# Optimization experiments

Hardware: AMD Instinct MI355X
Metric: run time of the kernel (lower is better)

Reference implementation:

```python
import jax, jax.numpy as jnp
import numpy as np

B, S, H = 2, 4096, 256
NH, NKV = 8, 4
HD = H // NH          # 32
GROUPS = NH // NKV    # 2
ROPE_BASE = 10000.0


def _rope_cos_sin(seq_len, dim, dtype):
    inv_freq = 1.0 / (ROPE_BASE ** (jnp.arange(0, dim, 2, dtype=jnp.float32) / dim))
    t = jnp.arange(seq_len, dtype=jnp.float32)
    freqs = jnp.outer(t, inv_freq)            # [S, dim/2]
    emb = jnp.concatenate([freqs, freqs], -1)  # [S, dim]
    return jnp.cos(emb).astype(dtype), jnp.sin(emb).astype(dtype)


def _rotate_half(x):
    x1, x2 = jnp.split(x, 2, axis=-1)
    return jnp.concatenate([-x2, x1], axis=-1)


def setup_inputs() -> dict:
    key = jax.random.key(0)
    k0, k1, k2, k3, k4 = jax.random.split(key, 5)
    return {
        "hidden_states": jax.random.normal(k0, (B, S, H), jnp.float32),
        "Wq": jax.random.normal(k1, (H, H), jnp.float32) * 0.02,
        "Wk": jax.random.normal(k2, (NKV * HD, H), jnp.float32) * 0.02,
        "Wv": jax.random.normal(k3, (NKV * HD, H), jnp.float32) * 0.02,
        "Wo": jax.random.normal(k4, (H, H), jnp.float32) * 0.02,
    }


def reference(hidden_states, Wq, Wk, Wv, Wo):
    b, s, _ = hidden_states.shape
    # projections (nn.Linear: x @ W.T)
    q = (hidden_states @ Wq.T).reshape(b, s, NH, HD).transpose(0, 2, 1, 3)   # [b,nh,s,hd]
    k = (hidden_states @ Wk.T).reshape(b, s, NKV, HD).transpose(0, 2, 1, 3)  # [b,nkv,s,hd]
    v = (hidden_states @ Wv.T).reshape(b, s, NKV, HD).transpose(0, 2, 1, 3)
    # RoPE
    cos, sin = _rope_cos_sin(s, HD, hidden_states.dtype)  # [s,hd]
    q = q * cos + _rotate_half(q) * sin
    k = k * cos + _rotate_half(k) * sin
    # GQA: repeat kv heads (repeat_interleave over head dim)
    k = jnp.repeat(k, GROUPS, axis=1)  # [b,nh,s,hd]
    v = jnp.repeat(v, GROUPS, axis=1)
    # scores + causal mask
    scores = jnp.einsum('bhqd,bhkd->bhqk', q, k) / jnp.sqrt(jnp.float32(HD)).astype(q.dtype)
    causal = jnp.triu(jnp.full((s, s), -jnp.inf, dtype=scores.dtype), k=1)
    scores = scores + causal
    attn = jax.nn.softmax(scores.astype(jnp.float32), axis=-1).astype(q.dtype)
    out = jnp.einsum('bhqk,bhkd->bhqd', attn, v)          # [b,nh,s,hd]
    out = out.transpose(0, 2, 1, 3).reshape(b, s, NH * HD)
    return out @ Wo.T
```

## Files before the change

kernel.cpp:

```cpp
#include <hip/hip_runtime.h>
#include <hip/hip_bf16.h>
#include <stdint.h>

#define NB 2
#define SEQ 4096
#define HID 256
#define NHEAD 8
#define NKVH 4
#define HDIM 32

typedef __bf16 bf16;
typedef __bf16 bf16x8 __attribute__((ext_vector_type(8)));
typedef float f32x4 __attribute__((ext_vector_type(4)));

static __device__ __forceinline__ uint16_t bfbits(float f) {
    bf16 h = (bf16)f;
    return __builtin_bit_cast(uint16_t, h);
}
static __device__ __forceinline__ uint32_t pack_bf16(float lo, float hi) {
    return (uint32_t)bfbits(lo) | ((uint32_t)bfbits(hi) << 16);
}
static __device__ __forceinline__ float fexp2(float x) {
#if __has_builtin(__builtin_amdgcn_exp2f)
    return __builtin_amdgcn_exp2f(x);
#else
    float r; asm("v_exp_f32 %0, %1" : "=v"(r) : "v"(x)); return r;
#endif
}
static __device__ __forceinline__ void gld_lds16(const void* g, void* l) {
    __builtin_amdgcn_global_load_lds(
        (const __attribute__((address_space(1))) void*)g,
        (__attribute__((address_space(3))) void*)l, 16, 0, 0);
}

__global__ __launch_bounds__(256) void to_bf16(
    const float* __restrict__ hs, const float* __restrict__ Wq,
    const float* __restrict__ Wk, const float* __restrict__ Wv,
    const float* __restrict__ Wo,
    bf16* __restrict__ hsb, bf16* __restrict__ Wb, bf16* __restrict__ Wob)
{
    size_t idx = ((size_t)blockIdx.x * 256 + threadIdx.x) * 8;
    const float* src; bf16* dst; size_t off;
    if (idx < 2097152)      { src = hs; dst = hsb;        off = idx; }
    else if (idx < 2162688) { src = Wq; dst = Wb;         off = idx - 2097152; }
    else if (idx < 2195456) { src = Wk; dst = Wb + 65536; off = idx - 2162688; }
    else if (idx < 2228224) { src = Wv; dst = Wb + 98304; off = idx - 2195456; }
    else                    { src = Wo; dst = Wob;        off = idx - 2228224; }
    float4 a = *(const float4*)&src[off];
    float4 b = *(const float4*)&src[off + 4];
    uint32_t u0 = pack_bf16(a.x, a.y);
    uint32_t u1 = pack_bf16(a.z, a.w);
    uint32_t u2 = pack_bf16(b.x, b.y);
    uint32_t u3 = pack_bf16(b.z, b.w);
    *(uint4*)&dst[off] = make_uint4(u0, u1, u2, u3);
}

__global__ __launch_bounds__(256, 2) void qkv2(
    const bf16* __restrict__ hsb, const bf16* __restrict__ Wb,
    bf16* __restrict__ qws, bf16* __restrict__ kws, bf16* __restrict__ vtws)
{
    __shared__ bf16 As[64 * 256];
    __shared__ bf16 Bs[64 * 256];
    const int t = threadIdx.x;
    const int wid = t >> 6, lane = t & 63;
    const int g = lane >> 4, c = lane & 15;
    const int n0 = blockIdx.x * 64;
    const int m0 = blockIdx.y * 64;

    {
        const int half = lane >> 5;
        const int seg = lane & 31;
        #pragma unroll
        for (int i = 0; i < 8; ++i) {
            const int row = (i * 4 + wid) * 2 + half;
            const int sseg = seg ^ (row & 7);
            gld_lds16(hsb + (size_t)(m0 + row) * 256 + sseg * 8,
                      (char*)As + wid * 1024 + i * 4096);
            gld_lds16(Wb + (size_t)(n0 + row) * 256 + sseg * 8,
                      (char*)Bs + wid * 1024 + i * 4096);
        }
    }
    __syncthreads();

    const f32x4 zf = {0.f, 0.f, 0.f, 0.f};
    f32x4 acc[4] = {zf, zf, zf, zf};
    const int r = wid * 16 + c;
    const int aBase = r * 512;
    const int s7 = c & 7;
    #pragma unroll
    for (int j = 0; j < 8; ++j) {
        const int so = ((4 * j + g) ^ s7) << 4;
        bf16x8 af = *(const bf16x8*)((const char*)As + aBase + so);
        #pragma unroll
        for (int nt = 0; nt < 4; ++nt) {
            bf16x8 bfr = *(const bf16x8*)((const char*)Bs + (nt * 16 + c) * 512 + so);
            acc[nt] = __builtin_amdgcn_mfma_f32_16x16x32_bf16(af, bfr, acc[nt], 0, 0, 0);
        }
    }

    const float qscale = 1.4426950408889634f * 0.17677669529663687f;
    const float invf = exp2f(-0.83048202372184f * (float)c);
    #pragma unroll
    for (int rr = 0; rr < 4; ++rr) {
        int m = m0 + wid * 16 + g * 4 + rr;
        int b = m >> 12, s = m & (SEQ - 1);
        float sn, cs;
        sincosf((float)s * invf, &sn, &cs);
        if (n0 < 256) {
            #pragma unroll
            for (int np = 0; np < 4; np += 2) {
                int h = (n0 + np * 16) >> 5;
                float x1 = acc[np][rr], x2 = acc[np + 1][rr];
                float y1 = (x1 * cs - x2 * sn) * qscale;
                float y2 = (x2 * cs + x1 * sn) * qscale;
                size_t base = ((size_t)(b * NHEAD + h) * SEQ + s) * HDIM;
                qws[base + c] = (bf16)y1;
                qws[base + 16 + c] = (bf16)y2;
            }
        } else if (n0 < 384) {
            #pragma unroll
            for (int np = 0; np < 4; np += 2) {
                int kh = (n0 - 256 + np * 16) >> 5;
                float x1 = acc[np][rr], x2 = acc[np + 1][rr];
                float y1 = x1 * cs - x2 * sn;
                float y2 = x2 * cs + x1 * sn;
                size_t base = ((size_t)(b * NKVH + kh) * SEQ + s) * HDIM;
                kws[base + c] = (bf16)y1;
                kws[base + 16 + c] = (bf16)y2;
            }
        } else {
            #pragma unroll
            for (int nt = 0; nt < 4; ++nt) {
                int ng = n0 + nt * 16 + c - 384;
                int vh = ng >> 5, d = ng & 31;
                vtws[((size_t)(b * NKVH + vh) * HDIM + d) * SEQ + s] = (bf16)acc[nt][rr];
            }
        }
    }
}

__global__ __launch_bounds__(256, 2) void attn_fwd(
    const bf16* __restrict__ qws, const bf16* __restrict__ kws,
    const bf16* __restrict__ vtws,
    float* __restrict__ Oa, float* __restrict__ Ob,
    float* __restrict__ la, float* __restrict__ lb)
{
    __shared__ bf16 Kb[2][64 * 32];
    __shared__ bf16 Vb[2][32 * 64];
    __shared__ float tr[4][16 * 33];
    const int t = threadIdx.x;
    const int w = t >> 6, lane = t & 63;
    const int g = lane >> 4, c = lane & 15;
    const int wg = blockIdx.x;
    const int h = wg & 7;
    const int rest = wg >> 3;
    const int half = rest & 1;
    const int r2 = rest >> 1;
    const int b = r2 & 1;
    const int T = 31 - (r2 >> 1);
    const int kvh = h >> 1;
    const bf16* Kg = kws + (size_t)(b * NKVH + kvh) * SEQ * HDIM;
    const bf16* Vg = vtws + (size_t)(b * NKVH + kvh) * HDIM * SEQ;
    const int cbase = half * (T + 1);
    const int nloc = T + 1;
    const int q0 = T * 128 + w * 32;
    const int d_w = 2 * T + (w >> 1);

    const bf16* Qb = qws + (size_t)(b * NHEAD + h) * SEQ * HDIM;
    bf16x8 qf0 = *(const bf16x8*)&Qb[(size_t)(q0 + c) * HDIM + g * 8];
    bf16x8 qf1 = *(const bf16x8*)&Qb[(size_t)(q0 + 16 + c) * HDIM + g * 8];

    const int sd = t >> 3, sseg = t & 7;
    const bf16* kg_t = Kg + t * 8;
    const bf16* vg_t = Vg + (size_t)sd * SEQ + (sseg ^ (sd & 7)) * 8;
    char* kl[2] = { (char*)&Kb[0][0] + w * 1024, (char*)&Kb[1][0] + w * 1024 };
    char* vl[2] = { (char*)&Vb[0][0] + w * 1024, (char*)&Vb[1][0] + w * 1024 };

    const int kperm = 8 * (c >> 2) + (c & 3);
    const int kro = kperm * 64 + g * 16;
    const int cx = c & 7;
    const int vro0 = c * 128, vro1 = (16 + c) * 128;

    const f32x4 zf = {0.f, 0.f, 0.f, 0.f};
    union { uint32_t u[4]; bf16x8 v; } onesf;
    onesf.u[0] = onesf.u[1] = onesf.u[2] = onesf.u[3] = 0x3F803F80u;

    f32x4 o00 = zf, o01 = zf, ol0 = zf;
    f32x4 o10 = zf, o11 = zf, ol1 = zf;

    gld_lds16(kg_t + (size_t)cbase * 2048, kl[0]);
    gld_lds16(vg_t + (size_t)cbase * 64, vl[0]);
    __syncthreads();

    #pragma unroll 1
    for (int s = 0; s < nloc; ++s) {
        const int ci = cbase + s;
        const int sn = s + 1;
        if (sn < nloc) {
            gld_lds16(kg_t + (size_t)(cbase + sn) * 2048, kl[sn & 1]);
            gld_lds16(vg_t + (size_t)(cbase + sn) * 64, vl[sn & 1]);
        }
        if (ci <= d_w) {
            const char* kbuf = (const char*)&Kb[s & 1][0];
            const char* vbuf = (const char*)&Vb[s & 1][0];

            bf16x8 kf0 = *(const bf16x8*)(kbuf + kro);
            bf16x8 kf1 = *(const bf16x8*)(kbuf + kro + 256);
            bf16x8 kf2 = *(const bf16x8*)(kbuf + kro + 2048);
            bf16x8 kf3 = *(const bf16x8*)(kbuf + kro + 2304);
            bf16x8 vf00 = *(const bf16x8*)(vbuf + vro0 + ((g ^ cx) << 4));
            bf16x8 vf01 = *(const bf16x8*)(vbuf + vro1 + ((g ^ cx) << 4));
            bf16x8 vf10 = *(const bf16x8*)(vbuf + vro0 + (((4 + g) ^ cx) << 4));
            bf16x8 vf11 = *(const bf16x8*)(vbuf + vro1 + (((4 + g) ^ cx) << 4));

            const bool diag = (ci == d_w);
            const int qbase = (w & 1) * 32 + c;

            {
                f32x4 st0 = __builtin_amdgcn_mfma_f32_16x16x32_bf16(kf0, qf0, zf, 0, 0, 0);
                f32x4 st1 = __builtin_amdgcn_mfma_f32_16x16x32_bf16(kf1, qf0, zf, 0, 0, 0);
                f32x4 st2 = __builtin_amdgcn_mfma_f32_16x16x32_bf16(kf2, qf0, zf, 0, 0, 0);
                f32x4 st3 = __builtin_amdgcn_mfma_f32_16x16x32_bf16(kf3, qf0, zf, 0, 0, 0);
                if (diag) {
                    const int qoff = qbase;
                    #pragma unroll
                    for (int rr = 0; rr < 4; ++rr) {
                        if (8 * g + rr > qoff)          st0[rr] = -1e30f;
                        if (8 * g + 4 + rr > qoff)      st1[rr] = -1e30f;
                        if (32 + 8 * g + rr > qoff)     st2[rr] = -1e30f;
                        if (32 + 8 * g + 4 + rr > qoff) st3[rr] = -1e30f;
                    }
                }
                float p00 = fexp2(st0[0]), p01 = fexp2(st0[1]), p02 = fexp2(st0[2]), p03 = fexp2(st0[3]);
                float p10 = fexp2(st1[0]), p11 = fexp2(st1[1]), p12 = fexp2(st1[2]), p13 = fexp2(st1[3]);
                float p20 = fexp2(st2[0]), p21 = fexp2(st2[1]), p22 = fexp2(st2[2]), p23 = fexp2(st2[3]);
                float p30 = fexp2(st3[0]), p31 = fexp2(st3[1]), p32 = fexp2(st3[2]), p33 = fexp2(st3[3]);
                union { uint32_t u[4]; bf16x8 v; } pb0, pb1;
                asm("v_cvt_pk_bf16_f32 %0, %1, %2" : "=v"(pb0.u[0]) : "v"(p00), "v"(p01));
                asm("v_cvt_pk_bf16_f32 %0, %1, %2" : "=v"(pb0.u[1]) : "v"(p02), "v"(p03));
                asm("v_cvt_pk_bf16_f32 %0, %1, %2" : "=v"(pb0.u[2]) : "v"(p10), "v"(p11));
                asm("v_cvt_pk_bf16_f32 %0, %1, %2" : "=v"(pb0.u[3]) : "v"(p12), "v"(p13));
                asm("v_cvt_pk_bf16_f32 %0, %1, %2" : "=v"(pb1.u[0]) : "v"(p20), "v"(p21));
                asm("v_cvt_pk_bf16_f32 %0, %1, %2" : "=v"(pb1.u[1]) : "v"(p22), "v"(p23));
                asm("v_cvt_pk_bf16_f32 %0, %1, %2" : "=v"(pb1.u[2]) : "v"(p30), "v"(p31));
                asm("v_cvt_pk_bf16_f32 %0, %1, %2" : "=v"(pb1.u[3]) : "v"(p32), "v"(p33));
                o00 = __builtin_amdgcn_mfma_f32_16x16x32_bf16(vf00, pb0.v, o00, 0, 0, 0);
                o01 = __builtin_amdgcn_mfma_f32_16x16x32_bf16(vf01, pb0.v, o01, 0, 0, 0);
                ol0 = __builtin_amdgcn_mfma_f32_16x16x32_bf16(onesf.v, pb0.v, ol0, 0, 0, 0);
                o00 = __builtin_amdgcn_mfma_f32_16x16x32_bf16(vf10, pb1.v, o00, 0, 0, 0);
                o01 = __builtin_amdgcn_mfma_f32_16x16x32_bf16(vf11, pb1.v, o01, 0, 0, 0);
                ol0 = __builtin_amdgcn_mfma_f32_16x16x32_bf16(onesf.v, pb1.v, ol0, 0, 0, 0);
            }
            {
                f32x4 st0 = __builtin_amdgcn_mfma_f32_16x16x32_bf16(kf0, qf1, zf, 0, 0, 0);
                f32x4 st1 = __builtin_amdgcn_mfma_f32_16x16x32_bf16(kf1, qf1, zf, 0, 0, 0);
                f32x4 st2 = __builtin_amdgcn_mfma_f32_16x16x32_bf16(kf2, qf1, zf, 0, 0, 0);
                f32x4 st3 = __builtin_amdgcn_mfma_f32_16x16x32_bf16(kf3, qf1, zf, 0, 0, 0);
                if (diag) {
                    const int qoff = qbase + 16;
                    #pragma unroll
                    for (int rr = 0; rr < 4; ++rr) {
                        if (8 * g + rr > qoff)          st0[rr] = -1e30f;
                        if (8 * g + 4 + rr > qoff)      st1[rr] = -1e30f;
                        if (32 + 8 * g + rr > qoff)     st2[rr] = -1e30f;
                        if (32 + 8 * g + 4 + rr > qoff) st3[rr] = -1e30f;
                    }
                }
                float p00 = fexp2(st0[0]), p01 = fexp2(st0[1]), p02 = fexp2(st0[2]), p03 = fexp2(st0[3]);
                float p10 = fexp2(st1[0]), p11 = fexp2(st1[1]), p12 = fexp2(st1[2]), p13 = fexp2(st1[3]);
                float p20 = fexp2(st2[0]), p21 = fexp2(st2[1]), p22 = fexp2(st2[2]), p23 = fexp2(st2[3]);
                float p30 = fexp2(st3[0]), p31 = fexp2(st3[1]), p32 = fexp2(st3[2]), p33 = fexp2(st3[3]);
                union { uint32_t u[4]; bf16x8 v; } pb0, pb1;
                asm("v_cvt_pk_bf16_f32 %0, %1, %2" : "=v"(pb0.u[0]) : "v"(p00), "v"(p01));
                asm("v_cvt_pk_bf16_f32 %0, %1, %2" : "=v"(pb0.u[1]) : "v"(p02), "v"(p03));
                asm("v_cvt_pk_bf16_f32 %0, %1, %2" : "=v"(pb0.u[2]) : "v"(p10), "v"(p11));
                asm("v_cvt_pk_bf16_f32 %0, %1, %2" : "=v"(pb0.u[3]) : "v"(p12), "v"(p13));
                asm("v_cvt_pk_bf16_f32 %0, %1, %2" : "=v"(pb1.u[0]) : "v"(p20), "v"(p21));
                asm("v_cvt_pk_bf16_f32 %0, %1, %2" : "=v"(pb1.u[1]) : "v"(p22), "v"(p23));
                asm("v_cvt_pk_bf16_f32 %0, %1, %2" : "=v"(pb1.u[2]) : "v"(p30), "v"(p31));
                asm("v_cvt_pk_bf16_f32 %0, %1, %2" : "=v"(pb1.u[3]) : "v"(p32), "v"(p33));
                o10 = __builtin_amdgcn_mfma_f32_16x16x32_bf16(vf00, pb0.v, o10, 0, 0, 0);
                o11 = __builtin_amdgcn_mfma_f32_16x16x32_bf16(vf01, pb0.v, o11, 0, 0, 0);
                ol1 = __builtin_amdgcn_mfma_f32_16x16x32_bf16(onesf.v, pb0.v, ol1, 0, 0, 0);
                o10 = __builtin_amdgcn_mfma_f32_16x16x32_bf16(vf10, pb1.v, o10, 0, 0, 0);
                o11 = __builtin_amdgcn_mfma_f32_16x16x32_bf16(vf11, pb1.v, o11, 0, 0, 0);
                ol1 = __builtin_amdgcn_mfma_f32_16x16x32_bf16(onesf.v, pb1.v, ol1, 0, 0, 0);
            }
        }
        __syncthreads();
    }

    #pragma unroll 1
    for (int j = 0; j < 2; ++j) {
        f32x4 a0 = j ? o10 : o00;
        f32x4 a1 = j ? o11 : o01;
        f32x4 al = j ? ol1 : ol0;
        #pragma unroll
        for (int rr = 0; rr < 4; ++rr) {
            tr[w][c * 33 + 4 * g + rr]      = a0[rr];
            tr[w][c * 33 + 16 + 4 * g + rr] = a1[rr];
        }
        float* Op = half ? Ob : Oa;
        float* lp = half ? lb : la;
        if (g == 0) lp[((size_t)b * SEQ + q0 + j * 16 + c) * 8 + h] = al[0];
        int q = lane >> 2, dp = (lane & 3) * 8;
        size_t m = (size_t)b * SEQ + q0 + j * 16 + q;
        float4 f0 = make_float4(tr[w][q * 33 + dp + 0], tr[w][q * 33 + dp + 1],
                                tr[w][q * 33 + dp + 2], tr[w][q * 33 + dp + 3]);
        float4 f1 = make_float4(tr[w][q * 33 + dp + 4], tr[w][q * 33 + dp + 5],
                                tr[w][q * 33 + dp + 6], tr[w][q * 33 + dp + 7]);
        *(float4*)&Op[m * HID + h * HDIM + dp]     = f0;
        *(float4*)&Op[m * HID + h * HDIM + dp + 4] = f1;
    }
}

__global__ __launch_bounds__(256) void combine(
    const float* __restrict__ Oa, const float* __restrict__ Ob,
    const float* __restrict__ la, const float* __restrict__ lb,
    bf16* __restrict__ att)
{
    const size_t e = ((size_t)blockIdx.x * 256 + threadIdx.x) * 8;
    const size_t m = e >> 8;
    const int hh = (int)(e & 255) >> 5;
    const float inv = 1.0f / (la[m * 8 + hh] + lb[m * 8 + hh]);
    float4 a0 = *(const float4*)&Oa[e];
    float4 a1 = *(const float4*)&Oa[e + 4];
    float4 b0 = *(const float4*)&Ob[e];
    float4 b1 = *(const float4*)&Ob[e + 4];
    uint32_t u0 = pack_bf16((a0.x + b0.x) * inv, (a0.y + b0.y) * inv);
    uint32_t u1 = pack_bf16((a0.z + b0.z) * inv, (a0.w + b0.w) * inv);
    uint32_t u2 = pack_bf16((a1.x + b1.x) * inv, (a1.y + b1.y) * inv);
    uint32_t u3 = pack_bf16((a1.z + b1.z) * inv, (a1.w + b1.w) * inv);
    *(uint4*)&att[e] = make_uint4(u0, u1, u2, u3);
}

__global__ __launch_bounds__(256, 2) void out_proj2(
    const bf16* __restrict__ att, const bf16* __restrict__ Wob,
    float* __restrict__ out)
{
    __shared__ bf16 As[64 * 256];
    __shared__ bf16 Bs[64 * 256];
    const int t = threadIdx.x;
    const int wid = t >> 6, lane = t & 63;
    const int g = lane >> 4, c = lane & 15;
    const int n0 = blockIdx.x * 64;
    const int m0 = blockIdx.y * 64;

    {
        const int half = lane >> 5;
        const int seg = lane & 31;
        #pragma unroll
        for (int i = 0; i < 8; ++i) {
            const int row = (i * 4 + wid) * 2 + half;
            const int sseg = seg ^ (row & 7);
            gld_lds16(att + (size_t)(m0 + row) * 256 + sseg * 8,
                      (char*)As + wid * 1024 + i * 4096);
            gld_lds16(Wob + (size_t)(n0 + row) * 256 + sseg * 8,
                      (char*)Bs + wid * 1024 + i * 4096);
        }
    }
    __syncthreads();

    const f32x4 zf = {0.f, 0.f, 0.f, 0.f};
    f32x4 acc[4] = {zf, zf, zf, zf};
    const int r = wid * 16 + c;
    const int aBase = r * 512;
    const int s7 = c & 7;
    #pragma unroll
    for (int j = 0; j < 8; ++j) {
        const int so = ((4 * j + g) ^ s7) << 4;
        bf16x8 af = *(const bf16x8*)((const char*)As + aBase + so);
        #pragma unroll
        for (int nt = 0; nt < 4; ++nt) {
            bf16x8 bfr = *(const bf16x8*)((const char*)Bs + (nt * 16 + c) * 512 + so);
            acc[nt] = __builtin_amdgcn_mfma_f32_16x16x32_bf16(af, bfr, acc[nt], 0, 0, 0);
        }
    }

    #pragma unroll
    for (int nt = 0; nt < 4; ++nt) {
        #pragma unroll
        for (int rr = 0; rr < 4; ++rr) {
            int m = m0 + wid * 16 + g * 4 + rr;
            out[(size_t)m * HID + n0 + nt * 16 + c] = acc[nt][rr];
        }
    }
}

extern "C" void kernel_launch(void* const* d_in, const int* in_sizes, int n_in,
                              void* d_out, int out_size, void* d_ws, size_t ws_size,
                              hipStream_t stream) {
    const float* hs = (const float*)d_in[0];
    const float* Wq = (const float*)d_in[1];
    const float* Wk = (const float*)d_in[2];
    const float* Wv = (const float*)d_in[3];
    const float* Wo = (const float*)d_in[4];
    char* ws = (char*)d_ws;
    bf16* qws  = (bf16*)(ws);
    bf16* kws  = (bf16*)(ws + 4194304);
    bf16* vtws = (bf16*)(ws + 6291456);
    bf16* att  = (bf16*)(ws + 8388608);
    float* Oa  = (float*)(ws + 12582912);
    float* Ob  = (float*)(ws + 20971520);
    float* la  = (float*)(ws + 29360128);
    float* lb  = (float*)(ws + 29622272);
    bf16* hsb  = (bf16*)(ws + 29884416);
    bf16* Wb   = (bf16*)(ws + 34078720);
    bf16* Wob  = (bf16*)(ws + 34340864);

    to_bf16<<<1120, 256, 0, stream>>>(hs, Wq, Wk, Wv, Wo, hsb, Wb, Wob);
    qkv2<<<dim3(8, 128), 256, 0, stream>>>(hsb, Wb, qws, kws, vtws);
    attn_fwd<<<1024, 256, 0, stream>>>(qws, kws, vtws, Oa, Ob, la, lb);
    combine<<<1024, 256, 0, stream>>>(Oa, Ob, la, lb, att);
    out_proj2<<<dim3(4, 128), 256, 0, stream>>>(att, Wob, (float*)d_out);
}
```

Measured before the change: 62.93 us.

## Use four-stage LDS ring and process two KV chunks per barrier in attention

Replaces the double-buffered K/V staging with a four-slot ring in a single 32KB shared buffer, prefetching two chunks ahead and processing two chunks per loop iteration so only one __syncthreads is paid per pair of chunks. The per-chunk compute is moved into a macro invoked twice per iteration. The epilogue transpose scratch now aliases the K region of the shared buffer. This deepens prefetch and halves barrier count at the cost of doubling LDS from 16KB to 32KB of K/V staging, which may reduce occupancy.

```diff
diff --git a/kernel.cpp b/kernel.cpp
--- a/kernel.cpp
+++ b/kernel.cpp
@@ -139,15 +139,99 @@
     }
 }
 
+#define ATT_CHUNK(CI, KBUF, VBUF)                                              \
+  do {                                                                         \
+    const char* kbuf = (KBUF);                                                 \
+    const char* vbuf = (VBUF);                                                 \
+    bf16x8 kf0 = *(const bf16x8*)(kbuf + kro);                                 \
+    bf16x8 kf1 = *(const bf16x8*)(kbuf + kro + 256);                           \
+    bf16x8 kf2 = *(const bf16x8*)(kbuf + kro + 2048);                          \
+    bf16x8 kf3 = *(const bf16x8*)(kbuf + kro + 2304);                          \
+    bf16x8 vf00 = *(const bf16x8*)(vbuf + vro0 + ((g ^ cx) << 4));             \
+    bf16x8 vf01 = *(const bf16x8*)(vbuf + vro1 + ((g ^ cx) << 4));             \
+    bf16x8 vf10 = *(const bf16x8*)(vbuf + vro0 + (((4 + g) ^ cx) << 4));       \
+    bf16x8 vf11 = *(const bf16x8*)(vbuf + vro1 + (((4 + g) ^ cx) << 4));       \
+    const bool diag = ((CI) == d_w);                                           \
+    const int qbase = (w & 1) * 32 + c;                                        \
+    {                                                                          \
+        f32x4 st0 = __builtin_amdgcn_mfma_f32_16x16x32_bf16(kf0, qf0, zf, 0, 0, 0); \
+        f32x4 st1 = __builtin_amdgcn_mfma_f32_16x16x32_bf16(kf1, qf0, zf, 0, 0, 0); \
+        f32x4 st2 = __builtin_amdgcn_mfma_f32_16x16x32_bf16(kf2, qf0, zf, 0, 0, 0); \
+        f32x4 st3 = __builtin_amdgcn_mfma_f32_16x16x32_bf16(kf3, qf0, zf, 0, 0, 0); \
+        if (diag) {                                                            \
+            const int qoff = qbase;                                            \
+            _Pragma("unroll")                                                  \
+            for (int rr = 0; rr < 4; ++rr) {                                   \
+                if (8 * g + rr > qoff)          st0[rr] = -1e30f;              \
+                if (8 * g + 4 + rr > qoff)      st1[rr] = -1e30f;              \
+                if (32 + 8 * g + rr > qoff)     st2[rr] = -1e30f;              \
+                if (32 + 8 * g + 4 + rr > qoff) st3[rr] = -1e30f;              \
+            }                                                                  \
+        }                                                                      \
+        float p00 = fexp2(st0[0]), p01 = fexp2(st0[1]), p02 = fexp2(st0[2]), p03 = fexp2(st0[3]); \
+        float p10 = fexp2(st1[0]), p11 = fexp2(st1[1]), p12 = fexp2(st1[2]), p13 = fexp2(st1[3]); \
+        float p20 = fexp2(st2[0]), p21 = fexp2(st2[1]), p22 = fexp2(st2[2]), p23 = fexp2(st2[3]); \
+        float p30 = fexp2(st3[0]), p31 = fexp2(st3[1]), p32 = fexp2(st3[2]), p33 = fexp2(st3[3]); \
+        union { uint32_t u[4]; bf16x8 v; } pb0, pb1;                           \
+        asm("v_cvt_pk_bf16_f32 %0, %1, %2" : "=v"(pb0.u[0]) : "v"(p00), "v"(p01)); \
+        asm("v_cvt_pk_bf16_f32 %0, %1, %2" : "=v"(pb0.u[1]) : "v"(p02), "v"(p03)); \
+        asm("v_cvt_pk_bf16_f32 %0, %1, %2" : "=v"(pb0.u[2]) : "v"(p10), "v"(p11)); \
+        asm("v_cvt_pk_bf16_f32 %0, %1, %2" : "=v"(pb0.u[3]) : "v"(p12), "v"(p13)); \
+        asm("v_cvt_pk_bf16_f32 %0, %1, %2" : "=v"(pb1.u[0]) : "v"(p20), "v"(p21)); \
+        asm("v_cvt_pk_bf16_f32 %0, %1, %2" : "=v"(pb1.u[1]) : "v"(p22), "v"(p23)); \
+        asm("v_cvt_pk_bf16_f32 %0, %1, %2" : "=v"(pb1.u[2]) : "v"(p30), "v"(p31)); \
+        asm("v_cvt_pk_bf16_f32 %0, %1, %2" : "=v"(pb1.u[3]) : "v"(p32), "v"(p33)); \
+        o00 = __builtin_amdgcn_mfma_f32_16x16x32_bf16(vf00, pb0.v, o00, 0, 0, 0); \
+        o01 = __builtin_amdgcn_mfma_f32_16x16x32_bf16(vf01, pb0.v, o01, 0, 0, 0); \
+        ol0 = __builtin_amdgcn_mfma_f32_16x16x32_bf16(onesf.v, pb0.v, ol0, 0, 0, 0); \
+        o00 = __builtin_amdgcn_mfma_f32_16x16x32_bf16(vf10, pb1.v, o00, 0, 0, 0); \
+        o01 = __builtin_amdgcn_mfma_f32_16x16x32_bf16(vf11, pb1.v, o01, 0, 0, 0); \
+        ol0 = __builtin_amdgcn_mfma_f32_16x16x32_bf16(onesf.v, pb1.v, ol0, 0, 0, 0); \
+    }                                                                          \
+    {                                                                          \
+        f32x4 st0 = __builtin_amdgcn_mfma_f32_16x16x32_bf16(kf0, qf1, zf, 0, 0, 0); \
+        f32x4 st1 = __builtin_amdgcn_mfma_f32_16x16x32_bf16(kf1, qf1, zf, 0, 0, 0); \
+        f32x4 st2 = __builtin_amdgcn_mfma_f32_16x16x32_bf16(kf2, qf1, zf, 0, 0, 0); \
+        f32x4 st3 = __builtin_amdgcn_mfma_f32_16x16x32_bf16(kf3, qf1, zf, 0, 0, 0); \
+        if (diag) {                                                            \
+            const int qoff = qbase + 16;                                       \
+            _Pragma("unroll")                                                  \
+            for (int rr = 0; rr < 4; ++rr) {                                   \
+                if (8 * g + rr > qoff)          st0[rr] = -1e30f;              \
+                if (8 * g + 4 + rr > qoff)      st1[rr] = -1e30f;              \
+                if (32 + 8 * g + rr > qoff)     st2[rr] = -1e30f;              \
+                if (32 + 8 * g + 4 + rr > qoff) st3[rr] = -1e30f;              \
+            }                                                                  \
+        }                                                                      \
+        float p00 = fexp2(st0[0]), p01 = fexp2(st0[1]), p02 = fexp2(st0[2]), p03 = fexp2(st0[3]); \
+        float p10 = fexp2(st1[0]), p11 = fexp2(st1[1]), p12 = fexp2(st1[2]), p13 = fexp2(st1[3]); \
+        float p20 = fexp2(st2[0]), p21 = fexp2(st2[1]), p22 = fexp2(st2[2]), p23 = fexp2(st2[3]); \
+        float p30 = fexp2(st3[0]), p31 = fexp2(st3[1]), p32 = fexp2(st3[2]), p33 = fexp2(st3[3]); \
+        union { uint32_t u[4]; bf16x8 v; } pb0, pb1;                           \
+        asm("v_cvt_pk_bf16_f32 %0, %1, %2" : "=v"(pb0.u[0]) : "v"(p00), "v"(p01)); \
+        asm("v_cvt_pk_bf16_f32 %0, %1, %2" : "=v"(pb0.u[1]) : "v"(p02), "v"(p03)); \
+        asm("v_cvt_pk_bf16_f32 %0, %1, %2" : "=v"(pb0.u[2]) : "v"(p10), "v"(p11)); \
+        asm("v_cvt_pk_bf16_f32 %0, %1, %2" : "=v"(pb0.u[3]) : "v"(p12), "v"(p13)); \
+        asm("v_cvt_pk_bf16_f32 %0, %1, %2" : "=v"(pb1.u[0]) : "v"(p20), "v"(p21)); \
+        asm("v_cvt_pk_bf16_f32 %0, %1, %2" : "=v"(pb1.u[1]) : "v"(p22), "v"(p23)); \
+        asm("v_cvt_pk_bf16_f32 %0, %1, %2" : "=v"(pb1.u[2]) : "v"(p30), "v"(p31)); \
+        asm("v_cvt_pk_bf16_f32 %0, %1, %2" : "=v"(pb1.u[3]) : "v"(p32), "v"(p33)); \
+        o10 = __builtin_amdgcn_mfma_f32_16x16x32_bf16(vf00, pb0.v, o10, 0, 0, 0); \
+        o11 = __builtin_amdgcn_mfma_f32_16x16x32_bf16(vf01, pb0.v, o11, 0, 0, 0); \
+        ol1 = __builtin_amdgcn_mfma_f32_16x16x32_bf16(onesf.v, pb0.v, ol1, 0, 0, 0); \
+        o10 = __builtin_amdgcn_mfma_f32_16x16x32_bf16(vf10, pb1.v, o10, 0, 0, 0); \
+        o11 = __builtin_amdgcn_mfma_f32_16x16x32_bf16(vf11, pb1.v, o11, 0, 0, 0); \
+        ol1 = __builtin_amdgcn_mfma_f32_16x16x32_bf16(onesf.v, pb1.v, ol1, 0, 0, 0); \
+    }                                                                          \
+  } while (0)
+
 __global__ __launch_bounds__(256, 2) void attn_fwd(
     const bf16* __restrict__ qws, const bf16* __restrict__ kws,
     const bf16* __restrict__ vtws,
     float* __restrict__ Oa, float* __restrict__ Ob,
     float* __restrict__ la, float* __restrict__ lb)
 {
-    __shared__ bf16 Kb[2][64 * 32];
-    __shared__ bf16 Vb[2][32 * 64];
-    __shared__ float tr[4][16 * 33];
+    __shared__ char smem[32768];
     const int t = threadIdx.x;
     const int w = t >> 6, lane = t & 63;
     const int g = lane >> 4, c = lane & 15;
@@ -173,8 +257,8 @@
     const int sd = t >> 3, sseg = t & 7;
     const bf16* kg_t = Kg + t * 8;
     const bf16* vg_t = Vg + (size_t)sd * SEQ + (sseg ^ (sd & 7)) * 8;
-    char* kl[2] = { (char*)&Kb[0][0] + w * 1024, (char*)&Kb[1][0] + w * 1024 };
-    char* vl[2] = { (char*)&Vb[0][0] + w * 1024, (char*)&Vb[1][0] + w * 1024 };
+    char* kl = smem + w * 1024;
+    char* vl = smem + 16384 + w * 1024;
 
     const int kperm = 8 * (c >> 2) + (c & 3);
     const int kro = kperm * 64 + g * 16;
@@ -188,108 +272,42 @@
     f32x4 o00 = zf, o01 = zf, ol0 = zf;
     f32x4 o10 = zf, o11 = zf, ol1 = zf;
 
-    gld_lds16(kg_t + (size_t)cbase * 2048, kl[0]);
-    gld_lds16(vg_t + (size_t)cbase * 64, vl[0]);
+    gld_lds16(kg_t + (size_t)cbase * 2048, kl);
+    gld_lds16(vg_t + (size_t)cbase * 64, vl);
+    if (1 < nloc) {
+        gld_lds16(kg_t + (size_t)(cbase + 1) * 2048, kl + 4096);
+        gld_lds16(vg_t + (size_t)(cbase + 1) * 64, vl + 4096);
+    }
     __syncthreads();
 
+    const int nit = (nloc + 1) >> 1;
     #pragma unroll 1
-    for (int s = 0; s < nloc; ++s) {
-        const int ci = cbase + s;
-        const int sn = s + 1;
-        if (sn < nloc) {
-            gld_lds16(kg_t + (size_t)(cbase + sn) * 2048, kl[sn & 1]);
-            gld_lds16(vg_t + (size_t)(cbase + sn) * 64, vl[sn & 1]);
-        }
-        if (ci <= d_w) {
-            const char* kbuf = (const char*)&Kb[s & 1][0];
-            const char* vbuf = (const char*)&Vb[s & 1][0];
-
-            bf16x8 kf0 = *(const bf16x8*)(kbuf + kro);
-            bf16x8 kf1 = *(const bf16x8*)(kbuf + kro + 256);
-            bf16x8 kf2 = *(const bf16x8*)(kbuf + kro + 2048);
-            bf16x8 kf3 = *(const bf16x8*)(kbuf + kro + 2304);
-            bf16x8 vf00 = *(const bf16x8*)(vbuf + vro0 + ((g ^ cx) << 4));
-            bf16x8 vf01 = *(const bf16x8*)(vbuf + vro1 + ((g ^ cx) << 4));
-            bf16x8 vf10 = *(const bf16x8*)(vbuf + vro0 + (((4 + g) ^ cx) << 4));
-            bf16x8 vf11 = *(const bf16x8*)(vbuf + vro1 + (((4 + g) ^ cx) << 4));
-
-            const bool diag = (ci == d_w);
-            const int qbase = (w & 1) * 32 + c;
-
-            {
-                f32x4 st0 = __builtin_amdgcn_mfma_f32_16x16x32_bf16(kf0, qf0, zf, 0, 0, 0);
-                f32x4 st1 = __builtin_amdgcn_mfma_f32_16x16x32_bf16(kf1, qf0, zf, 0, 0, 0);
-                f32x4 st2 = __builtin_amdgcn_mfma_f32_16x16x32_bf16(kf2, qf0, zf, 0, 0, 0);
-                f32x4 st3 = __builtin_amdgcn_mfma_f32_16x16x32_bf16(kf3, qf0, zf, 0, 0, 0);
-                if (diag) {
-                    const int qoff = qbase;
-                    #pragma unroll
-                    for (int rr = 0; rr < 4; ++rr) {
-                        if (8 * g + rr > qoff)          st0[rr] = -1e30f;
-                        if (8 * g + 4 + rr > qoff)      st1[rr] = -1e30f;
-                        if (32 + 8 * g + rr > qoff)     st2[rr] = -1e30f;
-                        if (32 + 8 * g + 4 + rr > qoff) st3[rr] = -1e30f;
-                    }
-                }
-                float p00 = fexp2(st0[0]), p01 = fexp2(st0[1]), p02 = fexp2(st0[2]), p03 = fexp2(st0[3]);
-                float p10 = fexp2(st1[0]), p11 = fexp2(st1[1]), p12 = fexp2(st1[2]), p13 = fexp2(st1[3]);
-                float p20 = fexp2(st2[0]), p21 = fexp2(st2[1]), p22 = fexp2(st2[2]), p23 = fexp2(st2[3]);
-                float p30 = fexp2(st3[0]), p31 = fexp2(st3[1]), p32 = fexp2(st3[2]), p33 = fexp2(st3[3]);
-                union { uint32_t u[4]; bf16x8 v; } pb0, pb1;
-                asm("v_cvt_pk_bf16_f32 %0, %1, %2" : "=v"(pb0.u[0]) : "v"(p00), "v"(p01));
-                asm("v_cvt_pk_bf16_f32 %0, %1, %2" : "=v"(pb0.u[1]) : "v"(p02), "v"(p03));
-                asm("v_cvt_pk_bf16_f32 %0, %1, %2" : "=v"(pb0.u[2]) : "v"(p10), "v"(p11));
-                asm("v_cvt_pk_bf16_f32 %0, %1, %2" : "=v"(pb0.u[3]) : "v"(p12), "v"(p13));
-                asm("v_cvt_pk_bf16_f32 %0, %1, %2" : "=v"(pb1.u[0]) : "v"(p20), "v"(p21));
-                asm("v_cvt_pk_bf16_f32 %0, %1, %2" : "=v"(pb1.u[1]) : "v"(p22), "v"(p23));
-                asm("v_cvt_pk_bf16_f32 %0, %1, %2" : "=v"(pb1.u[2]) : "v"(p30), "v"(p31));
-                asm("v_cvt_pk_bf16_f32 %0, %1, %2" : "=v"(pb1.u[3]) : "v"(p32), "v"(p33));
-                o00 = __builtin_amdgcn_mfma_f32_16x16x32_bf16(vf00, pb0.v, o00, 0, 0, 0);
-                o01 = __builtin_amdgcn_mfma_f32_16x16x32_bf16(vf01, pb0.v, o01, 0, 0, 0);
-                ol0 = __builtin_amdgcn_mfma_f32_16x16x32_bf16(onesf.v, pb0.v, ol0, 0, 0, 0);
-                o00 = __builtin_amdgcn_mfma_f32_16x16x32_bf16(vf10, pb1.v, o00, 0, 0, 0);
-                o01 = __builtin_amdgcn_mfma_f32_16x16x32_bf16(vf11, pb1.v, o01, 0, 0, 0);
-                ol0 = __builtin_amdgcn_mfma_f32_16x16x32_bf16(onesf.v, pb1.v, ol0, 0, 0, 0);
-            }
-            {
-                f32x4 st0 = __builtin_amdgcn_mfma_f32_16x16x32_bf16(kf0, qf1, zf, 0, 0, 0);
-                f32x4 st1 = __builtin_amdgcn_mfma_f32_16x16x32_bf16(kf1, qf1, zf, 0, 0, 0);
-                f32x4 st2 = __builtin_amdgcn_mfma_f32_16x16x32_bf16(kf2, qf1, zf, 0, 0, 0);
-                f32x4 st3 = __builtin_amdgcn_mfma_f32_16x16x32_bf16(kf3, qf1, zf, 0, 0, 0);
-                if (diag) {
-                    const int qoff = qbase + 16;
-                    #pragma unroll
-                    for (int rr = 0; rr < 4; ++rr) {
-                        if (8 * g + rr > qoff)          st0[rr] = -1e30f;
-                        if (8 * g + 4 + rr > qoff)      st1[rr] = -1e30f;
-                        if (32 + 8 * g + rr > qoff)     st2[rr] = -1e30f;
-                        if (32 + 8 * g + 4 + rr > qoff) st3[rr] = -1e30f;
-                    }
-                }
-                float p00 = fexp2(st0[0]), p01 = fexp2(st0[1]), p02 = fexp2(st0[2]), p03 = fexp2(st0[3]);
-                float p10 = fexp2(st1[0]), p11 = fexp2(st1[1]), p12 = fexp2(st1[2]), p13 = fexp2(st1[3]);
-                float p20 = fexp2(st2[0]), p21 = fexp2(st2[1]), p22 = fexp2(st2[2]), p23 = fexp2(st2[3]);
-                float p30 = fexp2(st3[0]), p31 = fexp2(st3[1]), p32 = fexp2(st3[2]), p33 = fexp2(st3[3]);
-                union { uint32_t u[4]; bf16x8 v; } pb0, pb1;
-                asm("v_cvt_pk_bf16_f32 %0, %1, %2" : "=v"(pb0.u[0]) : "v"(p00), "v"(p01));
-                asm("v_cvt_pk_bf16_f32 %0, %1, %2" : "=v"(pb0.u[1]) : "v"(p02), "v"(p03));
-                asm("v_cvt_pk_bf16_f32 %0, %1, %2" : "=v"(pb0.u[2]) : "v"(p10), "v"(p11));
-                asm("v_cvt_pk_bf16_f32 %0, %1, %2" : "=v"(pb0.u[3]) : "v"(p12), "v"(p13));
-                asm("v_cvt_pk_bf16_f32 %0, %1, %2" : "=v"(pb1.u[0]) : "v"(p20), "v"(p21));
-                asm("v_cvt_pk_bf16_f32 %0, %1, %2" : "=v"(pb1.u[1]) : "v"(p22), "v"(p23));
-                asm("v_cvt_pk_bf16_f32 %0, %1, %2" : "=v"(pb1.u[2]) : "v"(p30), "v"(p31));
-                asm("v_cvt_pk_bf16_f32 %0, %1, %2" : "=v"(pb1.u[3]) : "v"(p32), "v"(p33));
-                o10 = __builtin_amdgcn_mfma_f32_16x16x32_bf16(vf00, pb0.v, o10, 0, 0, 0);
-                o11 = __builtin_amdgcn_mfma_f32_16x16x32_bf16(vf01, pb0.v, o11, 0, 0, 0);
-                ol1 = __builtin_amdgcn_mfma_f32_16x16x32_bf16(onesf.v, pb0.v, ol1, 0, 0, 0);
-                o10 = __builtin_amdgcn_mfma_f32_16x16x32_bf16(vf10, pb1.v, o10, 0, 0, 0);
-                o11 = __builtin_amdgcn_mfma_f32_16x16x32_bf16(vf11, pb1.v, o11, 0, 0, 0);
-                ol1 = __builtin_amdgcn_mfma_f32_16x16x32_bf16(onesf.v, pb1.v, ol1, 0, 0, 0);
-            }
+    for (int it = 0; it < nit; ++it) {
+        const int s0 = 2 * it, s1 = s0 + 1;
+        if (s0 + 2 < nloc) {
+            gld_lds16(kg_t + (size_t)(cbase + s0 + 2) * 2048, kl + ((s0 + 2) & 3) * 4096);
+            gld_lds16(vg_t + (size_t)(cbase + s0 + 2) * 64, vl + ((s0 + 2) & 3) * 4096);
+        }
+        if (s1 + 2 < nloc) {
+            gld_lds16(kg_t + (size_t)(cbase + s1 + 2) * 2048, kl + ((s1 + 2) & 3) * 4096);
+            gld_lds16(vg_t + (size_t)(cbase + s1 + 2) * 64, vl + ((s1 + 2) & 3) * 4096);
+        }
+        const int ci0 = cbase + s0;
+        if (ci0 <= d_w) {
+            ATT_CHUNK(ci0, smem + (s0 & 3) * 4096 + 0,
+                           smem + 16384 + (s0 & 3) * 4096);
+        }
+        const int ci1 = cbase + s1;
+        if (s1 < nloc && ci1 <= d_w) {
+            ATT_CHUNK(ci1, smem + (s1 & 3) * 4096 + 0,
+                           smem + 16384 + (s1 & 3) * 4096);
         }
         __syncthreads();
     }
 
+    float* tr = (float*)(smem + w * 2112);
+    float* Op = half ? Ob : Oa;
+    float* lp = half ? lb : la;
     #pragma unroll 1
     for (int j = 0; j < 2; ++j) {
         f32x4 a0 = j ? o10 : o00;
@@ -297,18 +315,16 @@
         f32x4 al = j ? ol1 : ol0;
         #pragma unroll
         for (int rr = 0; rr < 4; ++rr) {
-            tr[w][c * 33 + 4 * g + rr]      = a0[rr];
-            tr[w][c * 33 + 16 + 4 * g + rr] = a1[rr];
-        }
-        float* Op = half ? Ob : Oa;
-        float* lp = half ? lb : la;
+            tr[c * 33 + 4 * g + rr]      = a0[rr];
+            tr[c * 33 + 16 + 4 * g + rr] = a1[rr];
+        }
         if (g == 0) lp[((size_t)b * SEQ + q0 + j * 16 + c) * 8 + h] = al[0];
         int q = lane >> 2, dp = (lane & 3) * 8;
         size_t m = (size_t)b * SEQ + q0 + j * 16 + q;
-        float4 f0 = make_float4(tr[w][q * 33 + dp + 0], tr[w][q * 33 + dp + 1],
-                                tr[w][q * 33 + dp + 2], tr[w][q * 33 + dp + 3]);
-        float4 f1 = make_float4(tr[w][q * 33 + dp + 4], tr[w][q * 33 + dp + 5],
-                                tr[w][q * 33 + dp + 6], tr[w][q * 33 + dp + 7]);
+        float4 f0 = make_float4(tr[q * 33 + dp + 0], tr[q * 33 + dp + 1],
+                                tr[q * 33 + dp + 2], tr[q * 33 + dp + 3]);
+        float4 f1 = make_float4(tr[q * 33 + dp + 4], tr[q * 33 + dp + 5],
+                                tr[q * 33 + dp + 6], tr[q * 33 + dp + 7]);
         *(float4*)&Op[m * HID + h * HDIM + dp]     = f0;
         *(float4*)&Op[m * HID + h * HDIM + dp + 4] = f1;
     }
```

After: 62.33 us. About the same (-0.9%).
